# Optimization experiments

Measured on AMD Instinct MI355X. Metric: run time of the kernel, lower is better.

Reference implementation:

```python
import jax, jax.numpy as jnp
import numpy as np
from jax.ops import segment_sum

N_NODES = 100000


def _gcn_layer(x, W, b, src, dst, n_nodes):
    # DGL GraphConv with norm='both': out = D_in^{-1/2} A D_out^{-1/2} x W + b
    # degrees clamped to min 1 (DGL behavior, handles zero-degree nodes)
    ones_e = jnp.ones(src.shape[0], dtype=x.dtype)
    deg_out = jnp.clip(segment_sum(ones_e, src, num_segments=n_nodes), 1.0)
    deg_in = jnp.clip(segment_sum(ones_e, dst, num_segments=n_nodes), 1.0)
    h = x * jax.lax.rsqrt(deg_out)[:, None]            # [N, F] source norm
    agg = segment_sum(h[src], dst, num_segments=n_nodes)  # [N, F] sum over in-edges
    agg = agg * jax.lax.rsqrt(deg_in)[:, None]          # dest norm
    return agg @ W + b


def setup_inputs() -> dict:
    key = jax.random.key(0)
    k1, k2, k3, k4, k5 = jax.random.split(key, 5)
    E = 1600000
    x = jax.random.normal(k1, (N_NODES, 128), dtype=jnp.float32)
    edge_src = jax.random.randint(k2, (E,), 0, N_NODES, dtype=jnp.int32)
    edge_dst = jax.random.randint(k3, (E,), 0, N_NODES, dtype=jnp.int32)
    W1 = jax.random.normal(k4, (128, 64), dtype=jnp.float32) * (1.0 / np.sqrt(128))
    b1 = jnp.zeros((64,), dtype=jnp.float32)
    W2 = jax.random.normal(k5, (64, 64), dtype=jnp.float32) * (1.0 / np.sqrt(64))
    b2 = jnp.zeros((64,), dtype=jnp.float32)
    return {"x": x, "edge_src": edge_src, "edge_dst": edge_dst,
            "W1": W1, "b1": b1, "W2": W2, "b2": b2}


def reference(x, edge_src, edge_dst, W1, b1, W2, b2):
    h = _gcn_layer(x, W1, b1, edge_src, edge_dst, N_NODES)
    h = jax.nn.relu(h)
    out = _gcn_layer(h, W2, b2, edge_src, edge_dst, N_NODES)
    return out
```

## Files before the change

kernel.cpp:

```cpp
#include <hip/hip_runtime.h>
#include <hip/hip_fp16.h>


static inline size_t align256(size_t x) { return (x + 255) & ~(size_t)255; }

#define BKT_SHIFT 8
#define BKT_W 256
#define MAX_NBK 400
#define CAP 5120
#define SC_BLOCKS 256
#define SC_THREADS 512

typedef _Float16 f16x8 __attribute__((ext_vector_type(8)));
typedef float f32x4 __attribute__((ext_vector_type(4)));

__global__ __launch_bounds__(SC_THREADS)
void scatter_atomic_kernel(const int* __restrict__ src, const int* __restrict__ dst,
                           int* __restrict__ gcnt_d, int* __restrict__ gcnt_s,
                           int* __restrict__ ebuf, unsigned char* __restrict__ sbuf,
                           int nbk, int E, int slice_len) {
    __shared__ int hd[MAX_NBK];
    __shared__ int hs[MAX_NBK];
    __shared__ int cur_d[MAX_NBK];
    __shared__ int cur_s[MAX_NBK];
    const int b = blockIdx.x;
    const int t = threadIdx.x;
    for (int i = t; i < nbk; i += SC_THREADS) { hd[i] = 0; hs[i] = 0; }
    __syncthreads();
    const int beg = b * slice_len;
    const int end = min(beg + slice_len, E);
    for (int i = beg + t; i < end; i += SC_THREADS) {
        atomicAdd(&hd[dst[i] >> BKT_SHIFT], 1);
        atomicAdd(&hs[src[i] >> BKT_SHIFT], 1);
    }
    __syncthreads();
    for (int i = t; i < nbk; i += SC_THREADS) {
        int c = hd[i];
        cur_d[i] = i * CAP + (c ? atomicAdd(&gcnt_d[i], c) : 0);
        c = hs[i];
        cur_s[i] = i * CAP + (c ? atomicAdd(&gcnt_s[i], c) : 0);
    }
    __syncthreads();
    for (int i = beg + t; i < end; i += SC_THREADS) {
        int d = dst[i], s = src[i];
        int pd = atomicAdd(&cur_d[d >> BKT_SHIFT], 1);
        ebuf[pd] = ((d & (BKT_W - 1)) << 17) | s;
        int ps = atomicAdd(&cur_s[s >> BKT_SHIFT], 1);
        sbuf[ps] = (unsigned char)(s & (BKT_W - 1));
    }
}

__global__ __launch_bounds__(256)
void bucket_csr_kernel(const int* __restrict__ ebuf,
                       const unsigned char* __restrict__ sbuf,
                       const int* __restrict__ gcnt_d, const int* __restrict__ gcnt_s,
                       int* __restrict__ csr_src,
                       int* __restrict__ cnt_in, int* __restrict__ cnt_out,
                       int* __restrict__ row_ptr,
                       int nbk, int N, int E) {
    __shared__ int cnt[BKT_W];
    __shared__ int rp[BKT_W];
    __shared__ int cur[BKT_W];
    __shared__ int cnts[BKT_W];
    __shared__ int red[256];
    __shared__ int sh_db;
    const int k = blockIdx.x;
    const int lo = k << BKT_SHIFT;
    const int span = min(BKT_W, N - lo);
    const int t = threadIdx.x;

    int s1 = 0;
    for (int i = t; i < k; i += 256) s1 += gcnt_d[i];
    red[t] = s1;
    __syncthreads();
    for (int off = 128; off >= 1; off >>= 1) {
        if (t < off) red[t] += red[t + off];
        __syncthreads();
    }
    if (t == 0) sh_db = red[0];
    __syncthreads();
    const int db = sh_db;
    const int eb = k * CAP, ee = eb + gcnt_d[k];
    const int sb = k * CAP, se = sb + gcnt_s[k];

    cnt[t] = 0; cnts[t] = 0;
    __syncthreads();
    for (int i = eb + t; i < ee; i += 256) atomicAdd(&cnt[ebuf[i] >> 17], 1);
    for (int i = sb + t; i < se; i += 256) atomicAdd(&cnts[sbuf[i]], 1);
    __syncthreads();
    rp[t] = cnt[t];
    __syncthreads();
    for (int off = 1; off < BKT_W; off <<= 1) {
        int v = (t >= off) ? rp[t - off] : 0;
        __syncthreads();
        rp[t] += v;
        __syncthreads();
    }
    if (t < span) {
        row_ptr[lo + t] = db + rp[t] - cnt[t];
        cnt_in[lo + t]  = cnt[t];
        cnt_out[lo + t] = cnts[t];
    }
    __syncthreads();
    cur[t] = db + rp[t] - cnt[t];
    __syncthreads();
    for (int i = eb + t; i < ee; i += 256) {
        int p = ebuf[i];
        int pos = atomicAdd(&cur[p >> 17], 1);
        csr_src[pos] = p & 0x1FFFF;
    }
    if (k == 0 && t == 0) row_ptr[N] = E;
}

template <int K>
__global__ __launch_bounds__(256)
void gemm_scale_kernel(const float* __restrict__ X, const float* __restrict__ W,
                       const int* __restrict__ cnt_out,
                       __half* __restrict__ Y, int N) {
    __shared__ _Float16 Wt[2][64][K + 8];
    const int t = threadIdx.x;
    for (int i = t; i < K * 64; i += 256) {
        const int k = i >> 6, j = i & 63;
        const float w = W[i];
        const _Float16 hi = (_Float16)w;
        Wt[0][j][k] = hi;
        Wt[1][j][k] = (_Float16)(w - (float)hi);
    }
    __syncthreads();

    const int wid  = t >> 6;
    const int lane = t & 63;
    const int col  = lane & 15;
    const int kg   = (lane >> 4) * 8;

    const int rowA = blockIdx.x * 64 + wid * 16 + col;
    const size_t xbase = (size_t)min(rowA, N - 1) * K;

    f32x4 acc0 = {}, acc1 = {}, acc2 = {}, acc3 = {};

#pragma unroll
    for (int ks = 0; ks < K; ks += 32) {
        float4 xa = *(const float4*)&X[xbase + ks + kg];
        float4 xb = *(const float4*)&X[xbase + ks + kg + 4];
        const float xs[8] = {xa.x, xa.y, xa.z, xa.w, xb.x, xb.y, xb.z, xb.w};
        f16x8 ahi, alo;
#pragma unroll
        for (int j = 0; j < 8; ++j) {
            const _Float16 h = (_Float16)xs[j];
            ahi[j] = h;
            alo[j] = (_Float16)(xs[j] - (float)h);
        }
#pragma unroll
        for (int tile = 0; tile < 4; ++tile) {
            const f16x8 bhi = *(const f16x8*)&Wt[0][col + 16 * tile][ks + kg];
            const f16x8 blo = *(const f16x8*)&Wt[1][col + 16 * tile][ks + kg];
            f32x4* acc = (tile == 0) ? &acc0 : (tile == 1) ? &acc1
                       : (tile == 2) ? &acc2 : &acc3;
            *acc = __builtin_amdgcn_mfma_f32_16x16x32_f16(ahi, bhi, *acc, 0, 0, 0);
            *acc = __builtin_amdgcn_mfma_f32_16x16x32_f16(alo, bhi, *acc, 0, 0, 0);
            *acc = __builtin_amdgcn_mfma_f32_16x16x32_f16(ahi, blo, *acc, 0, 0, 0);
        }
    }

    const int rbase = blockIdx.x * 64 + wid * 16 + (lane >> 4) * 4;
#pragma unroll
    for (int r = 0; r < 4; ++r) {
        const int rr = rbase + r;
        if (rr < N) {
            const float sc = rsqrtf((float)max(cnt_out[rr], 1));
            __half* yp = &Y[(size_t)rr * 64 + col];
            yp[0]  = __float2half_rn(acc0[r] * sc);
            yp[16] = __float2half_rn(acc1[r] * sc);
            yp[32] = __float2half_rn(acc2[r] * sc);
            yp[48] = __float2half_rn(acc3[r] * sc);
        }
    }
}

template <bool RELU>
__global__ __launch_bounds__(256)
void aggregate_kernel(const __half* __restrict__ Y,
                      const int* __restrict__ row_ptr,
                      const int* __restrict__ csr_src,
                      const int* __restrict__ cnt_in,
                      const float* __restrict__ bias,
                      float* __restrict__ out, int N) {
    const int n = blockIdx.x * 16 + (threadIdx.x >> 4);
    if (n >= N) return;
    const int fq = threadIdx.x & 15;

    const int start = row_ptr[n];
    const int end   = row_ptr[n + 1];
    const int last  = end - 1;

    float4 acc = {0.f, 0.f, 0.f, 0.f};
    for (int e = start; e < end; e += 12) {
        int idx[12];
#pragma unroll
        for (int j = 0; j < 12; ++j) idx[j] = csr_src[min(e + j, last)];
        uint2 v[12];
#pragma unroll
        for (int j = 0; j < 12; ++j)
            v[j] = *((const uint2*)(Y + ((size_t)idx[j] << 6)) + fq);
#pragma unroll
        for (int j = 0; j < 12; ++j) {
            if (e + j < end) {
                float2 a = __half22float2(*(const __half2*)&v[j].x);
                float2 b = __half22float2(*(const __half2*)&v[j].y);
                acc.x += a.x; acc.y += a.y; acc.z += b.x; acc.w += b.y;
            }
        }
    }

    const float sc = rsqrtf((float)max(cnt_in[n], 1));
    const float4 bb = *(const float4*)&bias[4 * fq];
    float4 o;
    o.x = acc.x * sc + bb.x;
    o.y = acc.y * sc + bb.y;
    o.z = acc.z * sc + bb.z;
    o.w = acc.w * sc + bb.w;
    if (RELU) {
        o.x = fmaxf(o.x, 0.f); o.y = fmaxf(o.y, 0.f);
        o.z = fmaxf(o.z, 0.f); o.w = fmaxf(o.w, 0.f);
    }
    *(float4*)&out[((size_t)n << 6) + 4 * fq] = o;
}

extern "C" void kernel_launch(void* const* d_in, const int* in_sizes, int n_in,
                              void* d_out, int out_size, void* d_ws, size_t ws_size,
                              hipStream_t stream) {
    const float* x   = (const float*)d_in[0];
    const int*   src = (const int*)d_in[1];
    const int*   dst = (const int*)d_in[2];
    const float* W1  = (const float*)d_in[3];
    const float* b1  = (const float*)d_in[4];
    const float* W2  = (const float*)d_in[5];
    const float* b2  = (const float*)d_in[6];
    float* out = (float*)d_out;

    const int N = in_sizes[0] / 128;
    const int E = in_sizes[1];

    const int nbk = (N + BKT_W - 1) >> BKT_SHIFT;

    char* ws = (char*)d_ws;
    size_t off = 0;
    __half* Y       = (__half*)(ws + off); off = align256(off + (size_t)N * 64 * sizeof(__half));
    int* csr_src    = (int*)(ws + off);    off = align256(off + (size_t)E * sizeof(int));
    int* ebuf       = (int*)(ws + off);    off = align256(off + (size_t)nbk * CAP * sizeof(int));
    unsigned char* sbuf = (unsigned char*)(ws + off); off = align256(off + (size_t)nbk * CAP);
    int* gcnt_d     = (int*)(ws + off);    off = align256(off + (size_t)nbk * sizeof(int));
    int* gcnt_s     = (int*)(ws + off);    off = align256(off + (size_t)nbk * sizeof(int));
    int* cnt_out    = (int*)(ws + off);    off = align256(off + (size_t)N * sizeof(int));
    int* cnt_in     = (int*)(ws + off);    off = align256(off + (size_t)N * sizeof(int));
    int* row_ptr    = (int*)(ws + off);    off = align256(off + (size_t)(N + 1) * sizeof(int));

    const int pslice = (E + SC_BLOCKS - 1) / SC_BLOCKS;

    hipMemsetAsync(gcnt_d, 0, (size_t)nbk * sizeof(int), stream);
    hipMemsetAsync(gcnt_s, 0, (size_t)nbk * sizeof(int), stream);
    scatter_atomic_kernel<<<SC_BLOCKS, SC_THREADS, 0, stream>>>(
        src, dst, gcnt_d, gcnt_s, ebuf, sbuf, nbk, E, pslice);
    bucket_csr_kernel<<<nbk, 256, 0, stream>>>(ebuf, sbuf, gcnt_d, gcnt_s, csr_src,
                                               cnt_in, cnt_out, row_ptr, nbk, N, E);

    const int gemm_blocks = (N + 63) / 64;
    const int agg_blocks  = (N + 15) / 16;

    gemm_scale_kernel<128><<<gemm_blocks, 256, 0, stream>>>(x, W1, cnt_out, Y, N);
    aggregate_kernel<true><<<agg_blocks, 256, 0, stream>>>(Y, row_ptr, csr_src, cnt_in, b1, out, N);

    gemm_scale_kernel<64><<<gemm_blocks, 256, 0, stream>>>(out, W2, cnt_out, Y, N);
    aggregate_kernel<false><<<agg_blocks, 256, 0, stream>>>(Y, row_ptr, csr_src, cnt_in, b2, out, N);
}
```

Measured before the change: 249.4 us.

## Fuse layer-1 aggregation with layer-2 GEMM and merge counter memsets

A new kernel aggregates the layer-1 neighbours, applies the norm, bias and ReLU, and stores the 16-node hidden tile in shared memory. It then multiplies that tile by W2 with split-precision fp16 MFMAs (hi/lo parts) and writes the scaled fp16 Y2. This drops one kernel launch and the fp32 round trip of the hidden activations through global memory, and it uses a separate Y2 buffer. Each block also reloads and transposes all of W2 into LDS, which adds per-block overhead, and the two bucket-counter memsets are merged into one.

```diff
diff --git a/kernel.cpp b/kernel.cpp
--- a/kernel.cpp
+++ b/kernel.cpp
@@ -177,6 +177,101 @@
     }
 }
 
+__global__ __launch_bounds__(256)
+void agg_gemm_kernel(const __half* __restrict__ Y,
+                     const int* __restrict__ row_ptr,
+                     const int* __restrict__ csr_src,
+                     const int* __restrict__ cnt_in,
+                     const int* __restrict__ cnt_out,
+                     const float* __restrict__ b1,
+                     const float* __restrict__ W2,
+                     __half* __restrict__ Y2, int N) {
+    __shared__ _Float16 Wt[2][64][72];
+    __shared__ _Float16 Hh[16][72];
+    __shared__ _Float16 Hl[16][72];
+    const int t = threadIdx.x;
+
+    for (int i = t; i < 64 * 64; i += 256) {
+        const int k = i >> 6, j = i & 63;
+        const float w = W2[i];
+        const _Float16 hi = (_Float16)w;
+        Wt[0][j][k] = hi;
+        Wt[1][j][k] = (_Float16)(w - (float)hi);
+    }
+
+    const int nl = t >> 4;
+    const int fq = t & 15;
+    const int n  = blockIdx.x * 16 + nl;
+    const int nc = min(n, N - 1);
+
+    const int start = row_ptr[nc];
+    const int end   = row_ptr[nc + 1];
+    const int last  = end - 1;
+
+    float4 acc = {0.f, 0.f, 0.f, 0.f};
+    for (int e = start; e < end; e += 12) {
+        int idx[12];
+#pragma unroll
+        for (int j = 0; j < 12; ++j) idx[j] = csr_src[min(e + j, last)];
+        uint2 v[12];
+#pragma unroll
+        for (int j = 0; j < 12; ++j)
+            v[j] = *((const uint2*)(Y + ((size_t)idx[j] << 6)) + fq);
+#pragma unroll
+        for (int j = 0; j < 12; ++j) {
+            if (e + j < end) {
+                float2 a = __half22float2(*(const __half2*)&v[j].x);
+                float2 b = __half22float2(*(const __half2*)&v[j].y);
+                acc.x += a.x; acc.y += a.y; acc.z += b.x; acc.w += b.y;
+            }
+        }
+    }
+
+    {
+        const float sc = rsqrtf((float)max(cnt_in[nc], 1));
+        const float4 bb = *(const float4*)&b1[4 * fq];
+        float hv[4];
+        hv[0] = fmaxf(acc.x * sc + bb.x, 0.f);
+        hv[1] = fmaxf(acc.y * sc + bb.y, 0.f);
+        hv[2] = fmaxf(acc.z * sc + bb.z, 0.f);
+        hv[3] = fmaxf(acc.w * sc + bb.w, 0.f);
+#pragma unroll
+        for (int q = 0; q < 4; ++q) {
+            const _Float16 hi = (_Float16)hv[q];
+            Hh[nl][4 * fq + q] = hi;
+            Hl[nl][4 * fq + q] = (_Float16)(hv[q] - (float)hi);
+        }
+    }
+    __syncthreads();
+
+    const int wid  = t >> 6;
+    const int lane = t & 63;
+    const int col  = lane & 15;
+    const int kg   = (lane >> 4) * 8;
+
+    f32x4 acc2 = {};
+#pragma unroll
+    for (int ks = 0; ks < 64; ks += 32) {
+        const f16x8 ahi = *(const f16x8*)&Hh[col][ks + kg];
+        const f16x8 alo = *(const f16x8*)&Hl[col][ks + kg];
+        const f16x8 bhi = *(const f16x8*)&Wt[0][16 * wid + col][ks + kg];
+        const f16x8 blo = *(const f16x8*)&Wt[1][16 * wid + col][ks + kg];
+        acc2 = __builtin_amdgcn_mfma_f32_16x16x32_f16(ahi, bhi, acc2, 0, 0, 0);
+        acc2 = __builtin_amdgcn_mfma_f32_16x16x32_f16(alo, bhi, acc2, 0, 0, 0);
+        acc2 = __builtin_amdgcn_mfma_f32_16x16x32_f16(ahi, blo, acc2, 0, 0, 0);
+    }
+
+    const int rloc = (lane >> 4) * 4;
+#pragma unroll
+    for (int r = 0; r < 4; ++r) {
+        const int rr = blockIdx.x * 16 + rloc + r;
+        if (rr < N) {
+            const float s2 = rsqrtf((float)max(cnt_out[rr], 1));
+            Y2[(size_t)rr * 64 + 16 * wid + col] = __float2half_rn(acc2[r] * s2);
+        }
+    }
+}
+
 template <bool RELU>
 __global__ __launch_bounds__(256)
 void aggregate_kernel(const __half* __restrict__ Y,
@@ -246,19 +341,20 @@
     char* ws = (char*)d_ws;
     size_t off = 0;
     __half* Y       = (__half*)(ws + off); off = align256(off + (size_t)N * 64 * sizeof(__half));
+    __half* Y2      = (__half*)(ws + off); off = align256(off + (size_t)N * 64 * sizeof(__half));
     int* csr_src    = (int*)(ws + off);    off = align256(off + (size_t)E * sizeof(int));
     int* ebuf       = (int*)(ws + off);    off = align256(off + (size_t)nbk * CAP * sizeof(int));
     unsigned char* sbuf = (unsigned char*)(ws + off); off = align256(off + (size_t)nbk * CAP);
-    int* gcnt_d     = (int*)(ws + off);    off = align256(off + (size_t)nbk * sizeof(int));
-    int* gcnt_s     = (int*)(ws + off);    off = align256(off + (size_t)nbk * sizeof(int));
+    int* gcnt       = (int*)(ws + off);    off = align256(off + (size_t)2 * nbk * sizeof(int));
+    int* gcnt_d     = gcnt;
+    int* gcnt_s     = gcnt + nbk;
     int* cnt_out    = (int*)(ws + off);    off = align256(off + (size_t)N * sizeof(int));
     int* cnt_in     = (int*)(ws + off);    off = align256(off + (size_t)N * sizeof(int));
     int* row_ptr    = (int*)(ws + off);    off = align256(off + (size_t)(N + 1) * sizeof(int));
 
     const int pslice = (E + SC_BLOCKS - 1) / SC_BLOCKS;
 
-    hipMemsetAsync(gcnt_d, 0, (size_t)nbk * sizeof(int), stream);
-    hipMemsetAsync(gcnt_s, 0, (size_t)nbk * sizeof(int), stream);
+    hipMemsetAsync(gcnt, 0, (size_t)2 * nbk * sizeof(int), stream);
     scatter_atomic_kernel<<<SC_BLOCKS, SC_THREADS, 0, stream>>>(
         src, dst, gcnt_d, gcnt_s, ebuf, sbuf, nbk, E, pslice);
     bucket_csr_kernel<<<nbk, 256, 0, stream>>>(ebuf, sbuf, gcnt_d, gcnt_s, csr_src,
@@ -268,8 +364,8 @@
     const int agg_blocks  = (N + 15) / 16;
 
     gemm_scale_kernel<128><<<gemm_blocks, 256, 0, stream>>>(x, W1, cnt_out, Y, N);
-    aggregate_kernel<true><<<agg_blocks, 256, 0, stream>>>(Y, row_ptr, csr_src, cnt_in, b1, out, N);
-
-    gemm_scale_kernel<64><<<gemm_blocks, 256, 0, stream>>>(out, W2, cnt_out, Y, N);
-    aggregate_kernel<false><<<agg_blocks, 256, 0, stream>>>(Y, row_ptr, csr_src, cnt_in, b2, out, N);
-}
+    agg_gemm_kernel<<<agg_blocks, 256, 0, stream>>>(Y, row_ptr, csr_src,
+                                                    cnt_in, cnt_out, b1, W2, Y2, N);
+    aggregate_kernel<false><<<agg_blocks, 256, 0, stream>>>(Y2, row_ptr, csr_src,
+                                                            cnt_in, b2, out, N);
+}
```

Result: no change. 245.4 us (-1.6%).
